# Kernel optimization log

Hardware: AMD Instinct MI355X
Metric: run time of the kernel (lower is better)

Reference implementation:

```python
import jax, jax.numpy as jnp
import numpy as np

B, T, C = 2, 2048, 1024
NH, H = 16, 64
FF = 3 * C  # feedforward_factor = 3
EPS = 1e-6


def setup_inputs() -> dict:
    key = jax.random.key(0)
    ks = jax.random.split(key, 12)
    s = lambda k, shape, fan: jax.random.normal(k, shape, jnp.float32) * (fan ** -0.5)
    return {
        "x":  jax.random.normal(ks[0], (B, T, C), jnp.float32),
        # per-head projections, stored [nh, C, H] (torch Linear weight [H,C] transposed)
        "Wq": s(ks[1], (NH, C, H), C),
        "Wk": s(ks[2], (NH, C, H), C),
        "Wv": s(ks[3], (NH, C, H), C),
        # combine_heads: torch Linear(nh*H -> C): weight [C, nh*H], bias [C]
        "Wo": s(ks[4], (C, NH * H), NH * H),
        "bo": jnp.zeros((C,), jnp.float32),
        # feedforward
        "W1": s(ks[5], (FF, C), C),
        "b1": jnp.zeros((FF,), jnp.float32),
        "W2": s(ks[6], (C, FF), FF),
        "b2": jnp.zeros((C,), jnp.float32),
        # layer norms (affine)
        "g1": jnp.ones((C,), jnp.float32),
        "be1": jnp.zeros((C,), jnp.float32),
        "g2": jnp.ones((C,), jnp.float32),
        "be2": jnp.zeros((C,), jnp.float32),
    }


def _layernorm(x, gamma, beta):
    # torch: mean / unbiased std (ddof=1), eps added to std (not variance)
    mean = jnp.mean(x, axis=-1, keepdims=True)
    std = jnp.std(x, axis=-1, keepdims=True, ddof=1)
    return gamma * (x - mean) / (std + EPS) + beta


def _attention(xn, Wq, Wk, Wv, Wo, bo):
    q = jnp.einsum("btc,hck->bhtk", xn, Wq)
    k = jnp.einsum("bsc,hck->bhsk", xn, Wk)
    v = jnp.einsum("bsc,hck->bhsk", xn, Wv)
    scores = jnp.einsum("bhtk,bhsk->bhts", q, k) / jnp.sqrt(jnp.float32(H))
    causal = jnp.tril(jnp.ones((T, T), dtype=bool))
    scores = jnp.where(causal, scores, -jnp.inf)
    attn = jax.nn.softmax(scores, axis=-1)
    ctx = jnp.einsum("bhts,bhsk->bhtk", attn, v)
    ctx = jnp.transpose(ctx, (0, 2, 1, 3)).reshape(xn.shape[0], T, NH * H)
    return ctx @ Wo.T + bo


def reference(x, Wq, Wk, Wv, Wo, bo, W1, b1, W2, b2, g1, be1, g2, be2):
    x = x + _attention(_layernorm(x, g1, be1), Wq, Wk, Wv, Wo, bo)
    h = _layernorm(x, g2, be2)
    x = x + (jax.nn.relu(h @ W1.T + b1) @ W2.T + b2)
    return x
```

## Files before the change

### kernel.cpp

```cpp
#include <hip/hip_runtime.h>
#include <stdint.h>

#define Tn   2048
#define Cn   1024
#define NHn  16
#define Hn   64
#define FFn  3072
#define Mrows 4096
#define LNEPS 1e-6f

#if __has_builtin(__builtin_amdgcn_exp2f)
#define EXP2(x) __builtin_amdgcn_exp2f(x)
#else
#define EXP2(x) exp2f(x)
#endif

typedef float f32x4 __attribute__((ext_vector_type(4)));
typedef __bf16 bf16x8 __attribute__((ext_vector_type(8)));
typedef unsigned short us8 __attribute__((ext_vector_type(8)));
typedef unsigned short us4 __attribute__((ext_vector_type(4)));
typedef unsigned int u32x4 __attribute__((ext_vector_type(4)));

__device__ __forceinline__ unsigned short f2bf(float f) {
    return __builtin_bit_cast(unsigned short, (__bf16)f);
}

__device__ __forceinline__ uint32_t pk2bf(float lo, float hi) {
    return (uint32_t)f2bf(lo) | ((uint32_t)f2bf(hi) << 16);
}

__device__ __forceinline__ void gl_lds16(const void* g, void* l) {
    __builtin_amdgcn_global_load_lds(
        (const __attribute__((address_space(1))) void*)g,
        (__attribute__((address_space(3))) void*)l, 16, 0, 0);
}

__global__ __launch_bounds__(256) void cast_qkv_kernel(
    const float* __restrict__ Wq, const float* __restrict__ Wk,
    const float* __restrict__ Wv, unsigned short* __restrict__ out)
{
    int idx = blockIdx.x * 256 + threadIdx.x;
    int n = idx >> 10, cc = idx & 1023;
    const float* W = (n < 1024) ? Wq : ((n < 2048) ? Wk : Wv);
    int nn = n & 1023;
    float v = W[(size_t)((nn >> 6) * 1024 + cc) * 64 + (nn & 63)];
    out[idx] = f2bf(v);
}

__global__ __launch_bounds__(256) void cast_w_kernel(
    const float* __restrict__ src, unsigned short* __restrict__ dst, int count)
{
    int idx = blockIdx.x * 256 + threadIdx.x;
    if (idx < count) dst[idx] = f2bf(src[idx]);
}

__global__ __launch_bounds__(256) void ln_kernel(
    const float* __restrict__ xin, const float* __restrict__ gamma,
    const float* __restrict__ beta, unsigned short* __restrict__ out)
{
    const int row = blockIdx.x;
    const int tid = threadIdx.x;
    const float4 v = ((const float4*)(xin + (size_t)row * Cn))[tid];
    float s  = v.x + v.y + v.z + v.w;
    float ss = v.x*v.x + v.y*v.y + v.z*v.z + v.w*v.w;
    #pragma unroll
    for (int off = 1; off < 64; off <<= 1) {
        s  += __shfl_xor(s, off);
        ss += __shfl_xor(ss, off);
    }
    __shared__ float red[8];
    const int wave = tid >> 6, lane = tid & 63;
    if (lane == 0) { red[wave] = s; red[4 + wave] = ss; }
    __syncthreads();
    float S  = red[0] + red[1] + red[2] + red[3];
    float SS = red[4] + red[5] + red[6] + red[7];
    float mean = S * (1.0f / 1024.0f);
    float var  = (SS - 1024.0f * mean * mean) * (1.0f / 1023.0f);
    var = fmaxf(var, 0.0f);
    float inv = 1.0f / (sqrtf(var) + LNEPS);
    const float4 gv = ((const float4*)gamma)[tid];
    const float4 bv = ((const float4*)beta)[tid];
    us4 ov;
    ov[0] = f2bf(gv.x * (v.x - mean) * inv + bv.x);
    ov[1] = f2bf(gv.y * (v.y - mean) * inv + bv.y);
    ov[2] = f2bf(gv.z * (v.z - mean) * inv + bv.z);
    ov[3] = f2bf(gv.w * (v.w - mean) * inv + bv.w);
    *(us4*)(out + (size_t)row * Cn + tid * 4) = ov;
}

template<int MODE>
__global__ __launch_bounds__(512) void gemm_bt(
    const unsigned short* __restrict__ A,
    const unsigned short* __restrict__ Bt,
    void* Cout,
    const float* __restrict__ bias,
    const float* resid,
    int M, int N, int K)
{
    __shared__ unsigned short lds[3][8192];
    const int tid  = threadIdx.x;
    const int wave = tid >> 6, lane = tid & 63;
    const int g = lane >> 4, c = lane & 15;
    const int wr = wave >> 2, wc = wave & 3;
    const int m0 = blockIdx.x * 128, n0 = blockIdx.y * 128;

    f32x4 acc[4][2];
    #pragma unroll
    for (int i = 0; i < 4; i++)
        #pragma unroll
        for (int j = 0; j < 2; j++) acc[i][j] = (f32x4){0.f, 0.f, 0.f, 0.f};

    const int srow = wave * 16 + (lane >> 2);
    const int scol = (lane & 3) * 8;
    const unsigned short* sA = A  + (size_t)(m0 + srow) * K + scol;
    const unsigned short* sB = Bt + (size_t)(n0 + srow) * K + scol;
    const int wdst = wave * 512;

    auto STAGE = [&](int t, int b) {
        const int ko = t * 32;
        gl_lds16(sA + ko, &lds[b][wdst]);
        gl_lds16(sB + ko, &lds[b][4096 + wdst]);
    };

    STAGE(0, 0);
    STAGE(1, 1);
    asm volatile("s_waitcnt vmcnt(2)" ::: "memory");
    __builtin_amdgcn_s_barrier();

    const int NT = K >> 5;
    int cur = 0;
    for (int t = 0; t < NT; ++t) {
        const bool pf = (t + 2 < NT);
        if (pf) { int b = cur + 2; if (b >= 3) b -= 3; STAGE(t + 2, b); }

        bf16x8 af[4], bfr[2];
        #pragma unroll
        for (int mi = 0; mi < 4; mi++)
            af[mi]  = *(const bf16x8*)&lds[cur][(wr * 64 + mi * 16 + c) * 32 + g * 8];
        #pragma unroll
        for (int ni = 0; ni < 2; ni++)
            bfr[ni] = *(const bf16x8*)&lds[cur][4096 + (wc * 32 + ni * 16 + c) * 32 + g * 8];
        __builtin_amdgcn_s_setprio(1);
        #pragma unroll
        for (int mi = 0; mi < 4; mi++)
            #pragma unroll
            for (int ni = 0; ni < 2; ni++)
                acc[mi][ni] = __builtin_amdgcn_mfma_f32_16x16x32_bf16(
                    af[mi], bfr[ni], acc[mi][ni], 0, 0, 0);
        __builtin_amdgcn_s_setprio(0);

        if (pf) asm volatile("s_waitcnt vmcnt(2)" ::: "memory");
        else    asm volatile("s_waitcnt vmcnt(0)" ::: "memory");
        __builtin_amdgcn_s_barrier();
        cur = (cur == 2) ? 0 : cur + 1;
    }

    const int rowb = m0 + wr * 64 + g * 4;
    const int colb = n0 + wc * 32 + c;
    #pragma unroll
    for (int mi = 0; mi < 4; mi++) {
        #pragma unroll
        for (int ni = 0; ni < 2; ni++) {
            const int col = colb + ni * 16;
            float bv = (MODE == 1 || MODE == 2) ? bias[col] : 0.f;
            #pragma unroll
            for (int r = 0; r < 4; r++) {
                const int row = rowb + mi * 16 + r;
                float v = acc[mi][ni][r];
                if (MODE == 1) {
                    float res = resid[(size_t)row * N + col];
                    ((float*)Cout)[(size_t)row * N + col] = v + bv + res;
                } else if (MODE == 2) {
                    float t = v + bv;
                    t = t > 0.f ? t : 0.f;
                    ((unsigned short*)Cout)[(size_t)row * N + col] = f2bf(t);
                } else {
                    ((unsigned short*)Cout)[(size_t)row * N + col] = f2bf(v);
                }
            }
        }
    }
}

__global__ __launch_bounds__(256) void transpose_v_kernel(
    const unsigned short* __restrict__ qkv, unsigned short* __restrict__ vt)
{
    __shared__ unsigned short tile[64][72];
    const int bh = blockIdx.y;
    const int b = bh >> 4, h = bh & 15;
    const int t0 = blockIdx.x * 64;
    const int tid = threadIdx.x;
    const int tr = tid >> 2;
    const int dc = (tid & 3) * 16;
    const unsigned short* src =
        qkv + (size_t)(b * Tn + t0 + tr) * 3072 + 2048 + h * 64 + dc;
    *(us8*)&tile[tr][dc]     = *(const us8*)src;
    *(us8*)&tile[tr][dc + 8] = *(const us8*)(src + 8);
    __syncthreads();
    const int dr = tid >> 2;
    const int tc = (tid & 3) * 16;
    unsigned short* dst = vt + (size_t)bh * Hn * Tn + (size_t)dr * Tn + t0 + tc;
    us8 o0, o1;
    #pragma unroll
    for (int e = 0; e < 8; e++) o0[e] = tile[tc + e][dr];
    #pragma unroll
    for (int e = 0; e < 8; e++) o1[e] = tile[tc + 8 + e][dr];
    *(us8*)dst       = o0;
    *(us8*)(dst + 8) = o1;
}

__global__ __launch_bounds__(256, 2) void attn_kernel(
    const unsigned short* __restrict__ qkv,
    const unsigned short* __restrict__ vt,
    unsigned short* __restrict__ ctx)
{
    const float SCL = 0.125f * 1.44269504088896f;
    const int tid  = threadIdx.x;
    const int wave = tid >> 6, lane = tid & 63;
    const int g = lane >> 4, c = lane & 15;
    const int pj = blockIdx.x * 4 + wave;
    const int bh = blockIdx.y;
    const int b = bh >> 4, h = bh & 15;
    const unsigned short* base  = qkv + (size_t)b * Tn * 3072;
    const unsigned short* qbase = base + h * 64;
    const unsigned short* kbase = base + 1024 + h * 64;
    const unsigned short* vtb   = vt + (size_t)bh * (Hn * Tn);

    for (int half = 0; half < 2; ++half) {
        const int tileIdx = half ? (63 - pj) : pj;
        const int t0 = tileIdx * 32;

        bf16x8 qf[2][2];
        #pragma unroll
        for (int qa = 0; qa < 2; qa++) {
            const unsigned short* qp = qbase + (size_t)(t0 + qa * 16 + c) * 3072 + g * 8;
            qf[qa][0] = *(const bf16x8*)qp;
            qf[qa][1] = *(const bf16x8*)(qp + 32);
        }

        float mrun[2] = {-1e30f, -1e30f};
        float lrun[2] = {0.f, 0.f};
        f32x4 o[2][4];
        #pragma unroll
        for (int qa = 0; qa < 2; qa++)
            #pragma unroll
            for (int nc = 0; nc < 4; nc++) o[qa][nc] = (f32x4){0.f, 0.f, 0.f, 0.f};

        for (int s0 = 0; s0 < t0 + 32; s0 += 64) {
            bf16x8 kf[4][2];
            #pragma unroll
            for (int sc = 0; sc < 4; sc++) {
                const unsigned short* kp = kbase + (size_t)(s0 + sc * 16 + c) * 3072 + g * 8;
                kf[sc][0] = *(const bf16x8*)kp;
                kf[sc][1] = *(const bf16x8*)(kp + 32);
            }
            bf16x8 vf[4][2];
            #pragma unroll
            for (int nc = 0; nc < 4; nc++)
                #pragma unroll
                for (int ks = 0; ks < 2; ks++)
                    vf[nc][ks] = *(const bf16x8*)(vtb + (size_t)(nc * 16 + c) * Tn
                                                  + s0 + ks * 32 + g * 8);

            f32x4 sacc[2][4];
            #pragma unroll
            for (int qa = 0; qa < 2; qa++)
                #pragma unroll
                for (int sc = 0; sc < 4; sc++) {
                    f32x4 z = (f32x4){0.f, 0.f, 0.f, 0.f};
                    z = __builtin_amdgcn_mfma_f32_16x16x32_bf16(kf[sc][0], qf[qa][0], z, 0, 0, 0);
                    z = __builtin_amdgcn_mfma_f32_16x16x32_bf16(kf[sc][1], qf[qa][1], z, 0, 0, 0);
                    sacc[qa][sc] = z;
                }

            uint32_t dw[2][4][2];
            #pragma unroll
            for (int qa = 0; qa < 2; qa++) {
                const int q = t0 + qa * 16 + c;
                float pm[4][4];
                const bool needMask = (s0 + 63 > t0 + qa * 16);
                #pragma unroll
                for (int sc = 0; sc < 4; sc++)
                    #pragma unroll
                    for (int r = 0; r < 4; r++) {
                        float v = sacc[qa][sc][r] * SCL;
                        if (needMask && (s0 + sc * 16 + 4 * g + r > q)) v = -1e30f;
                        pm[sc][r] = v;
                    }
                float tmax = pm[0][0];
                #pragma unroll
                for (int sc = 0; sc < 4; sc++)
                    #pragma unroll
                    for (int r = 0; r < 4; r++) tmax = fmaxf(tmax, pm[sc][r]);
                tmax = fmaxf(tmax, __shfl_xor(tmax, 16));
                tmax = fmaxf(tmax, __shfl_xor(tmax, 32));
                float mnew = fmaxf(mrun[qa], tmax);
                float corr = EXP2(mrun[qa] - mnew);
                mrun[qa] = mnew;
                float csum = 0.f;
                #pragma unroll
                for (int sc = 0; sc < 4; sc++)
                    #pragma unroll
                    for (int r = 0; r < 4; r++) {
                        float p = EXP2(pm[sc][r] - mnew);
                        pm[sc][r] = p;
                        csum += p;
                    }
                csum += __shfl_xor(csum, 16);
                csum += __shfl_xor(csum, 32);
                lrun[qa] = lrun[qa] * corr + csum;
                float cb[4];
                #pragma unroll
                for (int r = 0; r < 4; r++) cb[r] = __shfl(corr, 4 * g + r);
                #pragma unroll
                for (int nc = 0; nc < 4; nc++)
                    #pragma unroll
                    for (int r = 0; r < 4; r++) o[qa][nc][r] *= cb[r];
                #pragma unroll
                for (int sc = 0; sc < 4; sc++) {
                    dw[qa][sc][0] = pk2bf(pm[sc][0], pm[sc][1]);
                    dw[qa][sc][1] = pk2bf(pm[sc][2], pm[sc][3]);
                }
            }

            #pragma unroll
            for (int ks = 0; ks < 2; ks++) {
                #pragma unroll
                for (int qa = 0; qa < 2; qa++) {
                    u32x4 pd;
                    #pragma unroll
                    for (int jh = 0; jh < 2; jh++) {
                        const int srcLane = (2 * (g & 1) + jh) * 16 + c;
                        #pragma unroll
                        for (int hh = 0; hh < 2; hh++) {
                            int vA = __shfl((int)dw[qa][2 * ks][hh],     srcLane);
                            int vB = __shfl((int)dw[qa][2 * ks + 1][hh], srcLane);
                            pd[jh * 2 + hh] = (g < 2) ? (uint32_t)vA : (uint32_t)vB;
                        }
                    }
                    bf16x8 pa = __builtin_bit_cast(bf16x8, pd);
                    #pragma unroll
                    for (int nc = 0; nc < 4; nc++)
                        o[qa][nc] = __builtin_amdgcn_mfma_f32_16x16x32_bf16(
                            pa, vf[nc][ks], o[qa][nc], 0, 0, 0);
                }
            }
        }

        #pragma unroll
        for (int qa = 0; qa < 2; qa++) {
            float rl = 1.0f / lrun[qa];
            float lb[4];
            #pragma unroll
            for (int r = 0; r < 4; r++) lb[r] = __shfl(rl, 4 * g + r);
            #pragma unroll
            for (int nc = 0; nc < 4; nc++)
                #pragma unroll
                for (int r = 0; r < 4; r++) {
                    const int trow = t0 + qa * 16 + 4 * g + r;
                    ctx[(size_t)(b * Tn + trow) * 1024 + h * 64 + nc * 16 + c] =
                        f2bf(o[qa][nc][r] * lb[r]);
                }
        }
    }
}

extern "C" void kernel_launch(void* const* d_in, const int* in_sizes, int n_in,
                              void* d_out, int out_size, void* d_ws, size_t ws_size,
                              hipStream_t stream) {
    const float* x   = (const float*)d_in[0];
    const float* Wq  = (const float*)d_in[1];
    const float* Wk  = (const float*)d_in[2];
    const float* Wv  = (const float*)d_in[3];
    const float* Wo  = (const float*)d_in[4];
    const float* bo  = (const float*)d_in[5];
    const float* W1  = (const float*)d_in[6];
    const float* b1  = (const float*)d_in[7];
    const float* W2  = (const float*)d_in[8];
    const float* b2  = (const float*)d_in[9];
    const float* g1  = (const float*)d_in[10];
    const float* be1 = (const float*)d_in[11];
    const float* g2  = (const float*)d_in[12];
    const float* be2 = (const float*)d_in[13];

    char* ws = (char*)d_ws;
    unsigned short* wqkv = (unsigned short*)ws;  ws += (size_t)3072 * 1024 * 2;
    unsigned short* wo   = (unsigned short*)ws;  ws += (size_t)1024 * 1024 * 2;
    unsigned short* w1   = (unsigned short*)ws;  ws += (size_t)3072 * 1024 * 2;
    unsigned short* w2   = (unsigned short*)ws;  ws += (size_t)1024 * 3072 * 2;
    unsigned short* bufA = (unsigned short*)ws;  ws += (size_t)Mrows * 1024 * 2;
    unsigned short* bufB = (unsigned short*)ws;  ws += (size_t)Mrows * 3072 * 2;

    float* xout = (float*)d_out;
    unsigned short* vt = (unsigned short*)d_out;

    cast_qkv_kernel<<<12288, 256, 0, stream>>>(Wq, Wk, Wv, wqkv);
    cast_w_kernel<<<4096, 256, 0, stream>>>(Wo, wo, 1024 * 1024);
    cast_w_kernel<<<12288, 256, 0, stream>>>(W1, w1, 3072 * 1024);
    cast_w_kernel<<<12288, 256, 0, stream>>>(W2, w2, 1024 * 3072);

    ln_kernel<<<Mrows, 256, 0, stream>>>(x, g1, be1, bufA);
    gemm_bt<0><<<dim3(32, 24), 512, 0, stream>>>(bufA, wqkv, bufB, nullptr, nullptr,
                                                 Mrows, 3072, 1024);
    transpose_v_kernel<<<dim3(Tn / 64, 2 * NHn), 256, 0, stream>>>(bufB, vt);
    attn_kernel<<<dim3(8, 2 * NHn), 256, 0, stream>>>(bufB, vt, bufA);
    gemm_bt<1><<<dim3(32, 8), 512, 0, stream>>>(bufA, wo, xout, bo, x,
                                                Mrows, 1024, 1024);
    ln_kernel<<<Mrows, 256, 0, stream>>>(xout, g2, be2, bufA);
    gemm_bt<2><<<dim3(32, 24), 512, 0, stream>>>(bufA, w1, bufB, b1, nullptr,
                                                 Mrows, 3072, 1024);
    gemm_bt<1><<<dim3(32, 8), 512, 0, stream>>>(bufB, w2, xout, b2, (const float*)xout,
                                                Mrows, 1024, 3072);
}
```

Baseline: 258.8 us.

## Split attention KV range across two waves with LDS softmax merge

```diff
diff --git a/kernel.cpp b/kernel.cpp
--- a/kernel.cpp
+++ b/kernel.cpp
@@ -209,16 +209,20 @@
     *(us8*)(dst + 8) = o1;
 }
 
-__global__ __launch_bounds__(256, 2) void attn_kernel(
+__global__ __launch_bounds__(128, 2) void attn_kernel(
     const unsigned short* __restrict__ qkv,
     const unsigned short* __restrict__ vt,
     unsigned short* __restrict__ ctx)
 {
     const float SCL = 0.125f * 1.44269504088896f;
+    __shared__ float Osh[2][4][64][4];
+    __shared__ float Msh[2][64];
+    __shared__ float Lsh[2][64];
+
     const int tid  = threadIdx.x;
     const int wave = tid >> 6, lane = tid & 63;
     const int g = lane >> 4, c = lane & 15;
-    const int pj = blockIdx.x * 4 + wave;
+    const int pj = blockIdx.x;
     const int bh = blockIdx.y;
     const int b = bh >> 4, h = bh & 15;
     const unsigned short* base  = qkv + (size_t)b * Tn * 3072;
@@ -229,6 +233,10 @@
     for (int half = 0; half < 2; ++half) {
         const int tileIdx = half ? (63 - pj) : pj;
         const int t0 = tileIdx * 32;
+        const int nch  = (t0 + 95) >> 6;
+        const int nh0  = (nch + 1) >> 1;
+        const int cbeg = wave ? nh0 : 0;
+        const int cend = wave ? nch : nh0;
 
         bf16x8 qf[2][2];
         #pragma unroll
@@ -246,7 +254,8 @@
             #pragma unroll
             for (int nc = 0; nc < 4; nc++) o[qa][nc] = (f32x4){0.f, 0.f, 0.f, 0.f};
 
-        for (int s0 = 0; s0 < t0 + 32; s0 += 64) {
+        for (int ci = cbeg; ci < cend; ++ci) {
+            const int s0 = ci * 64;
             bf16x8 kf[4][2];
             #pragma unroll
             for (int sc = 0; sc < 4; sc++) {
@@ -347,21 +356,48 @@
             }
         }
 
-        #pragma unroll
-        for (int qa = 0; qa < 2; qa++) {
-            float rl = 1.0f / lrun[qa];
-            float lb[4];
-            #pragma unroll
-            for (int r = 0; r < 4; r++) lb[r] = __shfl(rl, 4 * g + r);
-            #pragma unroll
-            for (int nc = 0; nc < 4; nc++)
-                #pragma unroll
-                for (int r = 0; r < 4; r++) {
-                    const int trow = t0 + qa * 16 + 4 * g + r;
-                    ctx[(size_t)(b * Tn + trow) * 1024 + h * 64 + nc * 16 + c] =
-                        f2bf(o[qa][nc][r] * lb[r]);
-                }
-        }
+        f32x4 oS[4], oX[4];
+        float mS, lS, mX, lX;
+        if (wave == 0) {
+            #pragma unroll
+            for (int nc = 0; nc < 4; nc++) { oS[nc] = o[0][nc]; oX[nc] = o[1][nc]; }
+            mS = mrun[0]; lS = lrun[0]; mX = mrun[1]; lX = lrun[1];
+        } else {
+            #pragma unroll
+            for (int nc = 0; nc < 4; nc++) { oS[nc] = o[1][nc]; oX[nc] = o[0][nc]; }
+            mS = mrun[1]; lS = lrun[1]; mX = mrun[0]; lX = lrun[0];
+        }
+        #pragma unroll
+        for (int nc = 0; nc < 4; nc++)
+            *(f32x4*)&Osh[wave][nc][lane][0] = oX[nc];
+        Msh[wave][lane] = mX;
+        Lsh[wave][lane] = lX;
+        __syncthreads();
+        const int pw = wave ^ 1;
+        float mP = Msh[pw][lane];
+        float lP = Lsh[pw][lane];
+        float mM = fmaxf(mS, mP);
+        float cS = EXP2(mS - mM);
+        float cP = EXP2(mP - mM);
+        float rl = 1.0f / (lS * cS + lP * cP);
+        float cbS[4], cbP[4], lb[4];
+        #pragma unroll
+        for (int r = 0; r < 4; r++) {
+            cbS[r] = __shfl(cS, 4 * g + r);
+            cbP[r] = __shfl(cP, 4 * g + r);
+            lb[r]  = __shfl(rl, 4 * g + r);
+        }
+        #pragma unroll
+        for (int nc = 0; nc < 4; nc++) {
+            f32x4 oP = *(const f32x4*)&Osh[pw][nc][lane][0];
+            #pragma unroll
+            for (int r = 0; r < 4; r++) {
+                const int trow = t0 + wave * 16 + 4 * g + r;
+                float val = (oS[nc][r] * cbS[r] + oP[r] * cbP[r]) * lb[r];
+                ctx[(size_t)(b * Tn + trow) * 1024 + h * 64 + nc * 16 + c] = f2bf(val);
+            }
+        }
+        __syncthreads();
     }
 }
 
@@ -403,7 +439,7 @@
     gemm_bt<0><<<dim3(32, 24), 512, 0, stream>>>(bufA, wqkv, bufB, nullptr, nullptr,
                                                  Mrows, 3072, 1024);
     transpose_v_kernel<<<dim3(Tn / 64, 2 * NHn), 256, 0, stream>>>(bufB, vt);
-    attn_kernel<<<dim3(8, 2 * NHn), 256, 0, stream>>>(bufB, vt, bufA);
+    attn_kernel<<<dim3(32, 2 * NHn), 128, 0, stream>>>(bufB, vt, bufA);
     gemm_bt<1><<<dim3(32, 8), 512, 0, stream>>>(bufA, wo, xout, bo, x,
                                                 Mrows, 1024, 1024);
     ln_kernel<<<Mrows, 256, 0, stream>>>(xout, g2, be2, bufA);
```

Measured after the change: 264.8 us. 1.02x slower.
